# Kernel optimization log

Hardware: AMD Instinct MI355X
Metric: run time of the kernel (lower is better)

Reference implementation:

```python
import jax, jax.numpy as jnp
import numpy as np

N, E, MUL, HID = 50000, 400000, 32, 64


def setup_inputs() -> dict:
    key = jax.random.key(0)
    ks = jax.random.split(key, 16)
    inp = {
        'node_scalars': jax.random.normal(ks[0], (N, MUL), jnp.float32),
        'node_vectors': jax.random.normal(ks[1], (N, MUL, 3), jnp.float32),
        'sh': jax.random.normal(ks[2], (E, 4), jnp.float32),
        'norm': jax.random.uniform(ks[3], (E, 1), jnp.float32),
        'mlp_w1': jax.random.normal(ks[4], (1, HID), jnp.float32),
        'mlp_b1': jnp.zeros((HID,), jnp.float32),
        'mlp_w2': jax.random.normal(ks[5], (HID, HID), jnp.float32) / np.sqrt(HID),
        'mlp_b2': jnp.zeros((HID,), jnp.float32),
        'mlp_w3': jax.random.normal(ks[6], (HID, 4 * MUL), jnp.float32) / np.sqrt(HID),
        'mlp_b3': jnp.zeros((4 * MUL,), jnp.float32),
        'lin1_w_s': jax.random.normal(ks[7], (2 * MUL, 6 * MUL), jnp.float32),
        'lin1_w_v': jax.random.normal(ks[8], (2 * MUL, 2 * MUL), jnp.float32),
        'lin2_w_s': jax.random.normal(ks[9], (5 * MUL, MUL), jnp.float32),
        'lin2_w_v': jax.random.normal(ks[10], (3 * MUL, MUL), jnp.float32),
        'senders': jax.random.randint(ks[11], (E,), 0, N, jnp.int32),
        'receivers': jax.random.randint(ks[12], (E,), 0, N, jnp.int32),
    }
    return inp


def reference(node_scalars, node_vectors, sh, norm,
              mlp_w1, mlp_b1, mlp_w2, mlp_b2, mlp_w3, mlp_b3,
              lin1_w_s, lin1_w_v, lin2_w_s, lin2_w_v,
              senders, receivers):
    n = node_scalars.shape[0]
    y0, y1 = sh[:, :1], sh[:, 1:]                      # 0e SH [E,1], 1o SH [E,3]
    # ---- gather sender features ----
    s_e = node_scalars[senders]                         # [E,MUL]
    v_e = node_vectors[senders]                         # [E,MUL,3]
    # ---- CG tensor product (sh 0e+1o) x (MULx0e + MULx1o) -> 2MULx0e + 2MULx1o ----
    tp_s = jnp.concatenate([y0 * s_e,
                            jnp.einsum('ek,emk->em', y1, v_e) / jnp.sqrt(3.0)], axis=-1)   # [E,2MUL]
    tp_v = jnp.concatenate([y0[:, :, None] * v_e,
                            y1[:, None, :] * s_e[:, :, None]], axis=1)                      # [E,2MUL,3]
    # ---- MLP on edge norms -> one gating scalar per output irrep (4MUL) ----
    h = jax.nn.silu(norm @ mlp_w1 + mlp_b1)
    h = jax.nn.silu(h @ mlp_w2 + mlp_b2)
    scal = h @ mlp_w3 + mlp_b3                          # [E,4MUL]
    m2 = tp_s.shape[-1]
    tp_s = tp_s * scal[:, :m2]
    tp_v = tp_v * scal[:, m2:, None]
    # ---- scatter-mean into receivers ----
    cnt = jax.ops.segment_sum(jnp.ones((receivers.shape[0],), tp_s.dtype), receivers, num_segments=n)
    denom = jnp.maximum(cnt, 1.0)[:, None]
    agg_s = jax.ops.segment_sum(tp_s, receivers, num_segments=n) / denom                    # [N,2MUL]
    agg_v = jax.ops.segment_sum(tp_v, receivers, num_segments=n) / denom[:, :, None]        # [N,2MUL,3]
    # ---- equivariant Linear -> irreps + gate scalars ----
    x_s = agg_s @ lin1_w_s / jnp.sqrt(jnp.float32(agg_s.shape[-1]))                         # [N,6MUL]
    x_v = jnp.einsum('nmi,mo->noi', agg_v, lin1_w_v) / jnp.sqrt(jnp.float32(agg_v.shape[1]))# [N,2MUL,3]
    n_vec = x_v.shape[1]
    act_s = jax.nn.silu(x_s[:, : x_s.shape[-1] - n_vec])                                    # [N,4MUL]
    gates = jax.nn.sigmoid(x_s[:, x_s.shape[-1] - n_vec:])                                  # [N,2MUL]
    g_v = x_v * gates[:, :, None]
    # ---- concat skip + final Linear to output irreps (MULx0e + MULx1o) ----
    c_s = jnp.concatenate([act_s, node_scalars], axis=-1)                                   # [N,5MUL]
    c_v = jnp.concatenate([g_v, node_vectors], axis=1)                                      # [N,3MUL,3]
    o_s = c_s @ lin2_w_s / jnp.sqrt(jnp.float32(c_s.shape[-1]))                             # [N,MUL]
    o_v = jnp.einsum('nmi,mo->noi', c_v, lin2_w_v) / jnp.sqrt(jnp.float32(c_v.shape[1]))    # [N,MUL,3]
    return jnp.concatenate([o_s, o_v.reshape(o_v.shape[0], -1)], axis=-1)                   # [N,4MUL]
```

## Files before the change

### kernel.cpp

```cpp
#include <hip/hip_runtime.h>

#define NN 50000
#define NE 400000
#define NBINS 1024
#define NSBIN 512

#define RL1ST 0
#define RL1VT 12288
#define RL2S  16384
#define RL2V  21504
#define WTOT  24576

#define SLUT_N ((NBINS+1)*256)
#define INTS_N (3*NN + 1 + NE + 1024)
#define FIXED_FL ((size_t)WTOT + SLUT_N + INTS_N)

#define SCAN_B 196

#define S160 0.07905694150420949f
#define S96  0.10206207261596576f

__device__ __forceinline__ float sigf(float x){
  return __builtin_amdgcn_rcpf(1.0f + __expf(-x));
}
__device__ __forceinline__ float siluf(float x){ return x * sigf(x); }

__global__ __launch_bounds__(256) void convert_weights(
    const float* __restrict__ l1s, const float* __restrict__ l1v,
    const float* __restrict__ l2s, const float* __restrict__ l2v,
    float* __restrict__ wgt)
{
  int i = blockIdx.x*256 + threadIdx.x;
  if (i < 12288){ int o=i>>6, m=i&63; wgt[RL1ST + i] = l1s[m*192+o]; return; }
  if (i < 16384){ int t=i-12288; int o=t>>6, m=t&63; wgt[RL1VT + t] = l1v[m*64+o]; return; }
  if (i < 21504){ int t=i-16384; wgt[RL2S + t] = l2s[t]; return; }
  if (i < 24576){ int t=i-21504; wgt[RL2V + t] = l2v[t]; return; }
}

__global__ __launch_bounds__(128) void build_lut(
    const float* __restrict__ w1, const float* __restrict__ b1,
    const float* __restrict__ w2, const float* __restrict__ b2,
    const float* __restrict__ w3, const float* __restrict__ b3,
    float* __restrict__ slut)
{
  __shared__ float h1[64], h2[64], scal[128];
  int bin = blockIdx.x;
  float x = (float)bin / (float)NBINS;
  int t = threadIdx.x;
  if (t < 64) h1[t] = siluf(fmaf(x, w1[t], b1[t]));
  __syncthreads();
  if (t < 64){
    float a = b2[t];
    for (int k=0;k<64;k++) a = fmaf(h1[k], w2[k*64+t], a);
    h2[t] = siluf(a);
  }
  __syncthreads();
  {
    float a = b3[t];
    for (int k=0;k<64;k++) a = fmaf(h2[k], w3[k*128+t], a);
    scal[t] = a;
  }
  __syncthreads();
  for (int c=t; c<256; c+=128){
    int m=c>>3, q=c&7;
    int idx = (q==0)? m : (q==1)? (32+m) : (q<5)? (64+m) : (96+m);
    float v = scal[idx];
    if (q == 1) v *= 0.57735026918962576f;
    slut[(size_t)bin*256 + c] = v;
  }
}

__global__ __launch_bounds__(256) void count_kernel(
    const int* __restrict__ rcv, int* __restrict__ cnt)
{
  int e = blockIdx.x*256 + threadIdx.x;
  if (e < NE) atomicAdd(&cnt[rcv[e]], 1);
}

__global__ __launch_bounds__(256) void scan_a(
    const int* __restrict__ cnt, int* __restrict__ offs, int* __restrict__ bsum)
{
  __shared__ int sd[256];
  int tid = threadIdx.x;
  int i = blockIdx.x*256 + tid;
  int c = (i < NN) ? cnt[i] : 0;
  sd[tid] = c;
  __syncthreads();
  for (int off=1; off<256; off<<=1){
    int t = (tid >= off) ? sd[tid-off] : 0;
    __syncthreads();
    sd[tid] += t;
    __syncthreads();
  }
  if (i < NN) offs[i] = sd[tid] - c;
  if (tid == 255) bsum[blockIdx.x] = sd[255];
}

__global__ __launch_bounds__(256) void scan_b(
    const int* __restrict__ bsum, int* __restrict__ bbase, int* __restrict__ offs)
{
  __shared__ int sd[256];
  int tid = threadIdx.x;
  int v = (tid < SCAN_B) ? bsum[tid] : 0;
  sd[tid] = v;
  __syncthreads();
  for (int off=1; off<256; off<<=1){
    int t = (tid >= off) ? sd[tid-off] : 0;
    __syncthreads();
    sd[tid] += t;
    __syncthreads();
  }
  if (tid < SCAN_B) bbase[tid] = sd[tid] - v;
  if (tid == 255) offs[NN] = sd[255];
}

__global__ __launch_bounds__(256) void scan_c(
    const int* __restrict__ bbase, int* __restrict__ offs, int* __restrict__ curs)
{
  int i = blockIdx.x*256 + threadIdx.x;
  if (i < NN){
    int o = offs[i] + bbase[blockIdx.x];
    offs[i] = o;
    curs[i] = o;
  }
}

__global__ __launch_bounds__(256) void scatter_kernel(
    const int* __restrict__ rcv, int* __restrict__ curs, int* __restrict__ eids)
{
  int e = blockIdx.x*256 + threadIdx.x;
  if (e >= NE) return;
  int pos = atomicAdd(&curs[rcv[e]], 1);
  eids[pos] = e;
}

__global__ __launch_bounds__(256) void dhist_kernel(
    const int* __restrict__ offs, int* __restrict__ hist, int cn0, int cnn)
{
  __shared__ int lh[NSBIN];
  for (int j=threadIdx.x; j<NSBIN; j+=256) lh[j]=0;
  __syncthreads();
  int i = blockIdx.x*256 + threadIdx.x;
  if (i < cnn){
    int n = cn0 + i;
    int d = offs[n+1] - offs[n];
    int b = (d < NSBIN) ? (NSBIN-1-d) : 0;
    atomicAdd(&lh[b], 1);
  }
  __syncthreads();
  for (int j=threadIdx.x; j<NSBIN; j+=256){
    int v = lh[j];
    if (v) atomicAdd(&hist[j], v);
  }
}

__global__ __launch_bounds__(512) void dhist_scan(int* __restrict__ hist)
{
  __shared__ int sd[512];
  int t = threadIdx.x;
  int v = hist[t];
  sd[t] = v;
  __syncthreads();
  for (int off=1; off<512; off<<=1){
    int x = (t >= off) ? sd[t-off] : 0;
    __syncthreads();
    sd[t] += x;
    __syncthreads();
  }
  hist[t] = sd[t] - v;
}

__global__ __launch_bounds__(256) void dsort_kernel(
    const int* __restrict__ offs, int* __restrict__ hist,
    int* __restrict__ sorted, int cn0, int cnn)
{
  __shared__ int lh[NSBIN];
  __shared__ int lb[NSBIN];
  for (int j=threadIdx.x; j<NSBIN; j+=256) lh[j]=0;
  __syncthreads();
  int i = blockIdx.x*256 + threadIdx.x;
  int b = -1, rank = 0;
  if (i < cnn){
    int n = cn0 + i;
    int d = offs[n+1] - offs[n];
    b = (d < NSBIN) ? (NSBIN-1-d) : 0;
    rank = atomicAdd(&lh[b], 1);
  }
  __syncthreads();
  for (int j=threadIdx.x; j<NSBIN; j+=256){
    int v = lh[j];
    lb[j] = v ? atomicAdd(&hist[j], v) : 0;
  }
  __syncthreads();
  if (i < cnn) sorted[cn0 + lb[b] + rank] = cn0 + i;
}

__global__ __launch_bounds__(256) void edge_agg_kernel(
    const float* __restrict__ ns, const float* __restrict__ nv,
    const float* __restrict__ sh, const float* __restrict__ nrm,
    const int* __restrict__ snd,
    const int* __restrict__ offs, const int* __restrict__ eids,
    const int* __restrict__ sorted,
    const float* __restrict__ slut,
    float* __restrict__ agg, int cn0, int cnn)
{
  int wave = threadIdx.x >> 6;
  int lane = threadIdx.x & 63;
  int es = lane >> 5;
  int l  = lane & 31;
  int nls = blockIdx.x*4 + wave;
  if (nls >= cnn) return;
  int n = sorted[cn0 + nls];
  int p0 = offs[n], p1 = offs[n+1];
  const float4* slut4 = (const float4*)slut;
  float a0=0.f,a1=0.f,a2=0.f,a3=0.f,a4=0.f,a5=0.f,a6=0.f,a7=0.f;

  for (int base = p0; base < p1; base += 2){
    int p  = base + es;
    int pc = (p < p1) ? p : (p1 - 1);
    float ok = (p < p1) ? 1.0f : 0.0f;
    int e = eids[pc];
    int s = snd[e];
    float x = nrm[e];
    float4 y = *(const float4*)(sh + 4*e);

    float f = fminf(fmaxf(x*(float)NBINS, 0.0f), (float)NBINS - 0.001f);
    int b = (int)f;
    float tt = f - (float)b;
    const float4* Sp = slut4 + (size_t)b*64 + 2*l;
    float4 La = Sp[0];
    float4 Lb = Sp[1];
    float4 Lc = Sp[64];
    float4 Ld = Sp[65];

    float se = ns[(size_t)s*32 + l] * ok;
    const float* vp = nv + (size_t)s*96 + 3*l;
    float2 w = *(const float2*)vp;
    float v2 = vp[2];
    float v0 = w.x*ok, v1 = w.y*ok; v2 *= ok;

    float sc0 = fmaf(tt, Lc.x-La.x, La.x);
    float sc1 = fmaf(tt, Lc.y-La.y, La.y);
    float sc2 = fmaf(tt, Lc.z-La.z, La.z);
    float sc3 = fmaf(tt, Lc.w-La.w, La.w);
    float sc4 = fmaf(tt, Ld.x-Lb.x, Lb.x);
    float sc5 = fmaf(tt, Ld.y-Lb.y, Lb.y);
    float sc6 = fmaf(tt, Ld.z-Lb.z, Lb.z);
    float sc7 = fmaf(tt, Ld.w-Lb.w, Lb.w);

    float dot = fmaf(y.w, v2, fmaf(y.z, v1, y.y*v0));
    a0 = fmaf(y.x*se, sc0, a0);
    a1 = fmaf(dot,    sc1, a1);
    a2 = fmaf(y.x*v0, sc2, a2);
    a3 = fmaf(y.x*v1, sc3, a3);
    a4 = fmaf(y.x*v2, sc4, a4);
    a5 = fmaf(y.y*se, sc5, a5);
    a6 = fmaf(y.z*se, sc6, a6);
    a7 = fmaf(y.w*se, sc7, a7);
  }

  a0 += __shfl_xor(a0, 32); a1 += __shfl_xor(a1, 32);
  a2 += __shfl_xor(a2, 32); a3 += __shfl_xor(a3, 32);
  a4 += __shfl_xor(a4, 32); a5 += __shfl_xor(a5, 32);
  a6 += __shfl_xor(a6, 32); a7 += __shfl_xor(a7, 32);

  if (es == 0){
    int deg = p1 - p0;
    float inv = (deg > 0) ? __builtin_amdgcn_rcpf((float)deg) : 1.0f;
    float* ap = agg + (size_t)(n - cn0)*256;
    ap[l]       = a0*inv;
    ap[32+l]    = a1*inv;
    ap[64+l]    = a2*inv;
    ap[128+l]   = a3*inv;
    ap[192+l]   = a4*inv;
    ap[96+l]    = a5*inv;
    ap[160+l]   = a6*inv;
    ap[224+l]   = a7*inv;
  }
}

__global__ __launch_bounds__(256) __attribute__((amdgpu_waves_per_eu(3,8)))
void node_s_kernel(
    const float* __restrict__ ns, const float* __restrict__ wgt,
    const float* __restrict__ agg, int cn0, int cnn,
    float* __restrict__ out)
{
  __shared__ float red[3*64*33];
  int lane = threadIdx.x & 63, role = threadIdx.x >> 6;
  int ro = __builtin_amdgcn_readfirstlane(role);
  int nl = blockIdx.x*64 + lane;
  bool valid = (nl < cnn);
  int nls = valid ? nl : (cnn-1);
  int n = cn0 + nl;

  float aggs[64];
  float oacc[32];
  #pragma unroll
  for (int j=0;j<32;j++) oacc[j]=0.0f;

  {
    const float4* ar = (const float4*)(agg + (size_t)nls*256);
    #pragma unroll
    for (int g=0; g<16; g++){
      float4 v = ar[g];
      aggs[4*g+0]=v.x; aggs[4*g+1]=v.y; aggs[4*g+2]=v.z; aggs[4*g+3]=v.w;
    }
  }
  const float* l1sT = wgt + RL1ST + ro*32*64;
  const float* l2s  = wgt + RL2S;
  for (int t=0;t<32;t++){
    const float4* col = (const float4*)(l1sT + t*64);
    float d0=0,d1=0,d2=0,d3=0;
    #pragma unroll
    for (int j=0;j<16;j++){
      float4 c = col[j];
      d0 = fmaf(aggs[4*j+0], c.x, d0);
      d1 = fmaf(aggs[4*j+1], c.y, d1);
      d2 = fmaf(aggs[4*j+2], c.z, d2);
      d3 = fmaf(aggs[4*j+3], c.w, d3);
    }
    float act = siluf(((d0+d1)+(d2+d3))*0.125f);
    const float4* row = (const float4*)(l2s + (size_t)(ro*32 + t)*32);
    #pragma unroll
    for (int j=0;j<8;j++){
      float4 w = row[j];
      oacc[4*j+0] = fmaf(act, w.x, oacc[4*j+0]);
      oacc[4*j+1] = fmaf(act, w.y, oacc[4*j+1]);
      oacc[4*j+2] = fmaf(act, w.z, oacc[4*j+2]);
      oacc[4*j+3] = fmaf(act, w.w, oacc[4*j+3]);
    }
  }
  {
    const float4* sp = (const float4*)(ns + (size_t)(cn0+nls)*32 + ro*8);
    #pragma unroll
    for (int q4=0;q4<2;q4++){
      float4 v = sp[q4];
      float vv[4] = {v.x, v.y, v.z, v.w};
      #pragma unroll
      for (int u=0;u<4;u++){
        int q = ro*8 + q4*4 + u;
        const float4* row = (const float4*)(l2s + (size_t)(128+q)*32);
        #pragma unroll
        for (int j=0;j<8;j++){
          float4 w = row[j];
          oacc[4*j+0] = fmaf(vv[u], w.x, oacc[4*j+0]);
          oacc[4*j+1] = fmaf(vv[u], w.y, oacc[4*j+1]);
          oacc[4*j+2] = fmaf(vv[u], w.z, oacc[4*j+2]);
          oacc[4*j+3] = fmaf(vv[u], w.w, oacc[4*j+3]);
        }
      }
    }
  }

  if (role != 0){
    float* rp = red + (role-1)*(64*33) + lane*33;
    #pragma unroll
    for (int j=0;j<32;j++) rp[j] = oacc[j];
  }
  __syncthreads();
  if (role == 0 && valid){
    #pragma unroll
    for (int j=0;j<32;j++)
      oacc[j] += red[0*(64*33)+lane*33+j] + red[1*(64*33)+lane*33+j]
               + red[2*(64*33)+lane*33+j];
    float4* op = (float4*)(out + (size_t)n*128);
    #pragma unroll
    for (int j=0;j<8;j++){
      float4 o4;
      o4.x = oacc[4*j+0]*S160; o4.y = oacc[4*j+1]*S160;
      o4.z = oacc[4*j+2]*S160; o4.w = oacc[4*j+3]*S160;
      op[j] = o4;
    }
  }
}

__global__ __launch_bounds__(192) __attribute__((amdgpu_waves_per_eu(3,8)))
void node_v_kernel(
    const float* __restrict__ nv, const float* __restrict__ wgt,
    const float* __restrict__ agg, int cn0, int cnn,
    float* __restrict__ out)
{
  __shared__ float sw[64*97];
  int lane = threadIdx.x & 63, role = threadIdx.x >> 6;
  int ro = __builtin_amdgcn_readfirstlane(role);
  int nl = blockIdx.x*64 + lane;
  bool valid = (nl < cnn);
  int nls = valid ? nl : (cnn-1);
  const float* arow = agg + (size_t)nls*256;

  {
    float aggs[64];
    const float4* ar = (const float4*)arow;
    #pragma unroll
    for (int g=0; g<16; g++){
      float4 v = ar[g];
      aggs[4*g+0]=v.x; aggs[4*g+1]=v.y; aggs[4*g+2]=v.z; aggs[4*g+3]=v.w;
    }
    const float* l1g = wgt + RL1ST + 128*64;
    for (int o=ro; o<64; o+=3){
      const float4* col = (const float4*)(l1g + o*64);
      float d0=0,d1=0,d2=0,d3=0;
      #pragma unroll
      for (int j=0;j<16;j++){
        float4 c = col[j];
        d0 = fmaf(aggs[4*j+0], c.x, d0);
        d1 = fmaf(aggs[4*j+1], c.y, d1);
        d2 = fmaf(aggs[4*j+2], c.z, d2);
        d3 = fmaf(aggs[4*j+3], c.w, d3);
      }
      sw[o*64+lane] = sigf(((d0+d1)+(d2+d3))*0.125f);
    }
  }
  __syncthreads();

  int k = role;
  float aggv[64], oacc[32];
  #pragma unroll
  for (int j=0;j<32;j++) oacc[j]=0.0f;
  {
    const float4* av = (const float4*)(arow + 64 + 64*k);
    #pragma unroll
    for (int g=0; g<16; g++){
      float4 v = av[g];
      aggv[4*g+0]=v.x; aggv[4*g+1]=v.y; aggv[4*g+2]=v.z; aggv[4*g+3]=v.w;
    }
  }
  const float* l1vT = wgt + RL1VT;
  const float* l2v  = wgt + RL2V;
  for (int o=0;o<64;o++){
    const float4* col = (const float4*)(l1vT + o*64);
    float d0=0,d1=0,d2=0,d3=0;
    #pragma unroll
    for (int j=0;j<16;j++){
      float4 c = col[j];
      d0 = fmaf(aggv[4*j+0], c.x, d0);
      d1 = fmaf(aggv[4*j+1], c.y, d1);
      d2 = fmaf(aggv[4*j+2], c.z, d2);
      d3 = fmaf(aggv[4*j+3], c.w, d3);
    }
    float gv = (((d0+d1)+(d2+d3))*0.125f) * sw[o*64+lane];
    const float4* row = (const float4*)(l2v + (size_t)o*32);
    #pragma unroll
    for (int j=0;j<8;j++){
      float4 w = row[j];
      oacc[4*j+0] = fmaf(gv, w.x, oacc[4*j+0]);
      oacc[4*j+1] = fmaf(gv, w.y, oacc[4*j+1]);
      oacc[4*j+2] = fmaf(gv, w.z, oacc[4*j+2]);
      oacc[4*j+3] = fmaf(gv, w.w, oacc[4*j+3]);
    }
  }
  {
    const float* vp = nv + (size_t)(cn0+nls)*96 + k;
    #pragma unroll 8
    for (int q=0;q<32;q++){
      float a = vp[3*q];
      const float4* row = (const float4*)(l2v + (size_t)(64+q)*32);
      #pragma unroll
      for (int j=0;j<8;j++){
        float4 w = row[j];
        oacc[4*j+0] = fmaf(a, w.x, oacc[4*j+0]);
        oacc[4*j+1] = fmaf(a, w.y, oacc[4*j+1]);
        oacc[4*j+2] = fmaf(a, w.z, oacc[4*j+2]);
        oacc[4*j+3] = fmaf(a, w.w, oacc[4*j+3]);
      }
    }
  }

  __syncthreads();
  if (valid){
    #pragma unroll
    for (int j=0;j<32;j++) sw[lane*97 + 3*j + k] = oacc[j]*S96;
  }
  __syncthreads();
  int nb = blockIdx.x*64;
  #pragma unroll
  for (int r=0;r<8;r++){
    int F = r*192 + threadIdx.x;
    int i = F/24, j = F%24;
    if (nb + i < cnn){
      float4 o4;
      o4.x = sw[i*97 + 4*j + 0];
      o4.y = sw[i*97 + 4*j + 1];
      o4.z = sw[i*97 + 4*j + 2];
      o4.w = sw[i*97 + 4*j + 3];
      *(float4*)(out + (size_t)(cn0+nb+i)*128 + 32 + 4*j) = o4;
    }
  }
}

extern "C" void kernel_launch(void* const* d_in, const int* in_sizes, int n_in,
                              void* d_out, int out_size, void* d_ws, size_t ws_size,
                              hipStream_t stream) {
  const float* node_scalars = (const float*)d_in[0];
  const float* node_vectors = (const float*)d_in[1];
  const float* sh           = (const float*)d_in[2];
  const float* norm         = (const float*)d_in[3];
  const float* w1  = (const float*)d_in[4];
  const float* b1  = (const float*)d_in[5];
  const float* w2  = (const float*)d_in[6];
  const float* b2  = (const float*)d_in[7];
  const float* w3  = (const float*)d_in[8];
  const float* b3  = (const float*)d_in[9];
  const float* l1s = (const float*)d_in[10];
  const float* l1v = (const float*)d_in[11];
  const float* l2s = (const float*)d_in[12];
  const float* l2v = (const float*)d_in[13];
  const int* snd = (const int*)d_in[14];
  const int* rcv = (const int*)d_in[15];
  float* ws = (float*)d_ws;
  float* out = (float*)d_out;

  size_t ws_fl = ws_size / 4;
  if (ws_fl < FIXED_FL + 64*256) return;
  size_t aggcap = (ws_fl - FIXED_FL) / 256;
  int csize = (int)((aggcap < (size_t)NN) ? aggcap : (size_t)NN);
  int nchunks = (NN + csize - 1) / csize;

  float* wgt  = ws;
  float* slut = wgt + WTOT;
  int*   ib   = (int*)(slut + SLUT_N);
  int* offs   = ib;
  int* curs   = ib + NN + 1;
  int* eids   = ib + 2*NN + 1;
  int* sorted = ib + 2*NN + 1 + NE;
  int* cnt    = sorted;
  int* hist   = ib + 3*NN + 1 + NE;
  int* bsum   = hist + 512;
  int* bbase  = bsum + 256;
  float* agg  = (float*)(bbase + 256);

  hipMemsetAsync(cnt, 0, NN*sizeof(int), stream);

  convert_weights<<<(WTOT+255)/256, 256, 0, stream>>>(l1s, l1v, l2s, l2v, wgt);
  build_lut<<<NBINS+1, 128, 0, stream>>>(w1,b1,w2,b2,w3,b3, slut);

  count_kernel<<<(NE+255)/256, 256, 0, stream>>>(rcv, cnt);
  scan_a<<<SCAN_B, 256, 0, stream>>>(cnt, offs, bsum);
  scan_b<<<1, 256, 0, stream>>>(bsum, bbase, offs);
  scan_c<<<SCAN_B, 256, 0, stream>>>(bbase, offs, curs);
  scatter_kernel<<<(NE+255)/256, 256, 0, stream>>>(rcv, curs, eids);

  for (int ch = 0; ch < nchunks; ch++){
    int cn0 = ch * csize;
    int cnn = (NN - cn0 < csize) ? (NN - cn0) : csize;
    hipMemsetAsync(hist, 0, NSBIN*sizeof(int), stream);
    dhist_kernel<<<(cnn+255)/256, 256, 0, stream>>>(offs, hist, cn0, cnn);
    dhist_scan<<<1, 512, 0, stream>>>(hist);
    dsort_kernel<<<(cnn+255)/256, 256, 0, stream>>>(offs, hist, sorted, cn0, cnn);

    edge_agg_kernel<<<(cnn+3)/4, 256, 0, stream>>>(
        node_scalars, node_vectors, sh, norm, snd, offs, eids, sorted, slut,
        agg, cn0, cnn);
    node_s_kernel<<<(cnn+63)/64, 256, 0, stream>>>(
        node_scalars, wgt, agg, cn0, cnn, out);
    node_v_kernel<<<(cnn+63)/64, 192, 0, stream>>>(
        node_vectors, wgt, agg, cn0, cnn, out);
  }
}
```

Measured before the change: 354.2 us.

## Fuse node scalar and vector kernels into one 448-thread block kernel

Merges node_s_kernel and node_v_kernel into a single node_kernel where waves 0-3 handle the scalar path and waves 4-6 the vector path over the same 64 nodes. This removes one kernel launch per chunk and lets both paths share the agg rows in cache. The trade-off is larger per-block shared memory (red plus sw), changed occupancy bounds, and extra block-wide barriers that now make the scalar waves wait on the vector work. It also adds an unroll-2 pragma on the edge aggregation loop.

```diff
diff --git a/kernel.cpp b/kernel.cpp
--- a/kernel.cpp
+++ b/kernel.cpp
@@ -215,6 +215,7 @@
   const float4* slut4 = (const float4*)slut;
   float a0=0.f,a1=0.f,a2=0.f,a3=0.f,a4=0.f,a5=0.f,a6=0.f,a7=0.f;
 
+  #pragma unroll 2
   for (int base = p0; base < p1; base += 2){
     int p  = base + es;
     int pc = (p < p1) ? p : (p1 - 1);
@@ -279,126 +280,43 @@
   }
 }
 
-__global__ __launch_bounds__(256) __attribute__((amdgpu_waves_per_eu(3,8)))
-void node_s_kernel(
-    const float* __restrict__ ns, const float* __restrict__ wgt,
-    const float* __restrict__ agg, int cn0, int cnn,
-    float* __restrict__ out)
+__global__ __launch_bounds__(448) __attribute__((amdgpu_waves_per_eu(2,4)))
+void node_kernel(
+    const float* __restrict__ ns, const float* __restrict__ nv,
+    const float* __restrict__ wgt, const float* __restrict__ agg,
+    int cn0, int cnn, float* __restrict__ out)
 {
   __shared__ float red[3*64*33];
-  int lane = threadIdx.x & 63, role = threadIdx.x >> 6;
-  int ro = __builtin_amdgcn_readfirstlane(role);
+  __shared__ float sw[64*97];
+  int tid = threadIdx.x;
+  int wave = tid >> 6, lane = tid & 63;
+  bool isS = (wave < 4);
   int nl = blockIdx.x*64 + lane;
   bool valid = (nl < cnn);
   int nls = valid ? nl : (cnn-1);
   int n = cn0 + nl;
-
-  float aggs[64];
+  const float* arow = agg + (size_t)nls*256;
+  int kv = wave - 4;
+
   float oacc[32];
   #pragma unroll
   for (int j=0;j<32;j++) oacc[j]=0.0f;
 
-  {
-    const float4* ar = (const float4*)(agg + (size_t)nls*256);
-    #pragma unroll
-    for (int g=0; g<16; g++){
-      float4 v = ar[g];
-      aggs[4*g+0]=v.x; aggs[4*g+1]=v.y; aggs[4*g+2]=v.z; aggs[4*g+3]=v.w;
-    }
-  }
-  const float* l1sT = wgt + RL1ST + ro*32*64;
-  const float* l2s  = wgt + RL2S;
-  for (int t=0;t<32;t++){
-    const float4* col = (const float4*)(l1sT + t*64);
-    float d0=0,d1=0,d2=0,d3=0;
-    #pragma unroll
-    for (int j=0;j<16;j++){
-      float4 c = col[j];
-      d0 = fmaf(aggs[4*j+0], c.x, d0);
-      d1 = fmaf(aggs[4*j+1], c.y, d1);
-      d2 = fmaf(aggs[4*j+2], c.z, d2);
-      d3 = fmaf(aggs[4*j+3], c.w, d3);
-    }
-    float act = siluf(((d0+d1)+(d2+d3))*0.125f);
-    const float4* row = (const float4*)(l2s + (size_t)(ro*32 + t)*32);
-    #pragma unroll
-    for (int j=0;j<8;j++){
-      float4 w = row[j];
-      oacc[4*j+0] = fmaf(act, w.x, oacc[4*j+0]);
-      oacc[4*j+1] = fmaf(act, w.y, oacc[4*j+1]);
-      oacc[4*j+2] = fmaf(act, w.z, oacc[4*j+2]);
-      oacc[4*j+3] = fmaf(act, w.w, oacc[4*j+3]);
-    }
-  }
-  {
-    const float4* sp = (const float4*)(ns + (size_t)(cn0+nls)*32 + ro*8);
-    #pragma unroll
-    for (int q4=0;q4<2;q4++){
-      float4 v = sp[q4];
-      float vv[4] = {v.x, v.y, v.z, v.w};
-      #pragma unroll
-      for (int u=0;u<4;u++){
-        int q = ro*8 + q4*4 + u;
-        const float4* row = (const float4*)(l2s + (size_t)(128+q)*32);
-        #pragma unroll
-        for (int j=0;j<8;j++){
-          float4 w = row[j];
-          oacc[4*j+0] = fmaf(vv[u], w.x, oacc[4*j+0]);
-          oacc[4*j+1] = fmaf(vv[u], w.y, oacc[4*j+1]);
-          oacc[4*j+2] = fmaf(vv[u], w.z, oacc[4*j+2]);
-          oacc[4*j+3] = fmaf(vv[u], w.w, oacc[4*j+3]);
-        }
-      }
-    }
-  }
-
-  if (role != 0){
-    float* rp = red + (role-1)*(64*33) + lane*33;
-    #pragma unroll
-    for (int j=0;j<32;j++) rp[j] = oacc[j];
-  }
-  __syncthreads();
-  if (role == 0 && valid){
-    #pragma unroll
-    for (int j=0;j<32;j++)
-      oacc[j] += red[0*(64*33)+lane*33+j] + red[1*(64*33)+lane*33+j]
-               + red[2*(64*33)+lane*33+j];
-    float4* op = (float4*)(out + (size_t)n*128);
-    #pragma unroll
-    for (int j=0;j<8;j++){
-      float4 o4;
-      o4.x = oacc[4*j+0]*S160; o4.y = oacc[4*j+1]*S160;
-      o4.z = oacc[4*j+2]*S160; o4.w = oacc[4*j+3]*S160;
-      op[j] = o4;
-    }
-  }
-}
-
-__global__ __launch_bounds__(192) __attribute__((amdgpu_waves_per_eu(3,8)))
-void node_v_kernel(
-    const float* __restrict__ nv, const float* __restrict__ wgt,
-    const float* __restrict__ agg, int cn0, int cnn,
-    float* __restrict__ out)
-{
-  __shared__ float sw[64*97];
-  int lane = threadIdx.x & 63, role = threadIdx.x >> 6;
-  int ro = __builtin_amdgcn_readfirstlane(role);
-  int nl = blockIdx.x*64 + lane;
-  bool valid = (nl < cnn);
-  int nls = valid ? nl : (cnn-1);
-  const float* arow = agg + (size_t)nls*256;
-
-  {
+  if (isS){
+    int ro = __builtin_amdgcn_readfirstlane(wave);
     float aggs[64];
-    const float4* ar = (const float4*)arow;
-    #pragma unroll
-    for (int g=0; g<16; g++){
-      float4 v = ar[g];
-      aggs[4*g+0]=v.x; aggs[4*g+1]=v.y; aggs[4*g+2]=v.z; aggs[4*g+3]=v.w;
-    }
-    const float* l1g = wgt + RL1ST + 128*64;
-    for (int o=ro; o<64; o+=3){
-      const float4* col = (const float4*)(l1g + o*64);
+    {
+      const float4* ar = (const float4*)arow;
+      #pragma unroll
+      for (int g=0; g<16; g++){
+        float4 v = ar[g];
+        aggs[4*g+0]=v.x; aggs[4*g+1]=v.y; aggs[4*g+2]=v.z; aggs[4*g+3]=v.w;
+      }
+    }
+    const float* l1sT = wgt + RL1ST + ro*32*64;
+    const float* l2s  = wgt + RL2S;
+    for (int t=0;t<32;t++){
+      const float4* col = (const float4*)(l1sT + t*64);
       float d0=0,d1=0,d2=0,d3=0;
       #pragma unroll
       for (int j=0;j<16;j++){
@@ -408,74 +326,149 @@
         d2 = fmaf(aggs[4*j+2], c.z, d2);
         d3 = fmaf(aggs[4*j+3], c.w, d3);
       }
-      sw[o*64+lane] = sigf(((d0+d1)+(d2+d3))*0.125f);
-    }
-  }
-  __syncthreads();
-
-  int k = role;
-  float aggv[64], oacc[32];
-  #pragma unroll
-  for (int j=0;j<32;j++) oacc[j]=0.0f;
-  {
-    const float4* av = (const float4*)(arow + 64 + 64*k);
-    #pragma unroll
-    for (int g=0; g<16; g++){
-      float4 v = av[g];
-      aggv[4*g+0]=v.x; aggv[4*g+1]=v.y; aggv[4*g+2]=v.z; aggv[4*g+3]=v.w;
-    }
-  }
-  const float* l1vT = wgt + RL1VT;
-  const float* l2v  = wgt + RL2V;
-  for (int o=0;o<64;o++){
-    const float4* col = (const float4*)(l1vT + o*64);
-    float d0=0,d1=0,d2=0,d3=0;
-    #pragma unroll
-    for (int j=0;j<16;j++){
-      float4 c = col[j];
-      d0 = fmaf(aggv[4*j+0], c.x, d0);
-      d1 = fmaf(aggv[4*j+1], c.y, d1);
-      d2 = fmaf(aggv[4*j+2], c.z, d2);
-      d3 = fmaf(aggv[4*j+3], c.w, d3);
-    }
-    float gv = (((d0+d1)+(d2+d3))*0.125f) * sw[o*64+lane];
-    const float4* row = (const float4*)(l2v + (size_t)o*32);
-    #pragma unroll
-    for (int j=0;j<8;j++){
-      float4 w = row[j];
-      oacc[4*j+0] = fmaf(gv, w.x, oacc[4*j+0]);
-      oacc[4*j+1] = fmaf(gv, w.y, oacc[4*j+1]);
-      oacc[4*j+2] = fmaf(gv, w.z, oacc[4*j+2]);
-      oacc[4*j+3] = fmaf(gv, w.w, oacc[4*j+3]);
-    }
-  }
-  {
-    const float* vp = nv + (size_t)(cn0+nls)*96 + k;
-    #pragma unroll 8
-    for (int q=0;q<32;q++){
-      float a = vp[3*q];
-      const float4* row = (const float4*)(l2v + (size_t)(64+q)*32);
+      float act = siluf(((d0+d1)+(d2+d3))*0.125f);
+      const float4* row = (const float4*)(l2s + (size_t)(ro*32 + t)*32);
       #pragma unroll
       for (int j=0;j<8;j++){
         float4 w = row[j];
-        oacc[4*j+0] = fmaf(a, w.x, oacc[4*j+0]);
-        oacc[4*j+1] = fmaf(a, w.y, oacc[4*j+1]);
-        oacc[4*j+2] = fmaf(a, w.z, oacc[4*j+2]);
-        oacc[4*j+3] = fmaf(a, w.w, oacc[4*j+3]);
-      }
-    }
-  }
-
-  __syncthreads();
-  if (valid){
+        oacc[4*j+0] = fmaf(act, w.x, oacc[4*j+0]);
+        oacc[4*j+1] = fmaf(act, w.y, oacc[4*j+1]);
+        oacc[4*j+2] = fmaf(act, w.z, oacc[4*j+2]);
+        oacc[4*j+3] = fmaf(act, w.w, oacc[4*j+3]);
+      }
+    }
+    {
+      const float4* sp = (const float4*)(ns + (size_t)(cn0+nls)*32 + ro*8);
+      #pragma unroll
+      for (int q4=0;q4<2;q4++){
+        float4 v = sp[q4];
+        float vv[4] = {v.x, v.y, v.z, v.w};
+        #pragma unroll
+        for (int u=0;u<4;u++){
+          int q = ro*8 + q4*4 + u;
+          const float4* row = (const float4*)(l2s + (size_t)(128+q)*32);
+          #pragma unroll
+          for (int j=0;j<8;j++){
+            float4 w = row[j];
+            oacc[4*j+0] = fmaf(vv[u], w.x, oacc[4*j+0]);
+            oacc[4*j+1] = fmaf(vv[u], w.y, oacc[4*j+1]);
+            oacc[4*j+2] = fmaf(vv[u], w.z, oacc[4*j+2]);
+            oacc[4*j+3] = fmaf(vv[u], w.w, oacc[4*j+3]);
+          }
+        }
+      }
+    }
+    if (wave != 0){
+      float* rp = red + (wave-1)*(64*33) + lane*33;
+      #pragma unroll
+      for (int j=0;j<32;j++) rp[j] = oacc[j];
+    }
+  } else {
+    int ro = __builtin_amdgcn_readfirstlane(kv);
+    float aggs[64];
+    {
+      const float4* ar = (const float4*)arow;
+      #pragma unroll
+      for (int g=0; g<16; g++){
+        float4 v = ar[g];
+        aggs[4*g+0]=v.x; aggs[4*g+1]=v.y; aggs[4*g+2]=v.z; aggs[4*g+3]=v.w;
+      }
+    }
+    const float* l1g = wgt + RL1ST + 128*64;
+    for (int o=ro; o<64; o+=3){
+      const float4* col = (const float4*)(l1g + o*64);
+      float d0=0,d1=0,d2=0,d3=0;
+      #pragma unroll
+      for (int j=0;j<16;j++){
+        float4 c = col[j];
+        d0 = fmaf(aggs[4*j+0], c.x, d0);
+        d1 = fmaf(aggs[4*j+1], c.y, d1);
+        d2 = fmaf(aggs[4*j+2], c.z, d2);
+        d3 = fmaf(aggs[4*j+3], c.w, d3);
+      }
+      sw[o*64+lane] = sigf(((d0+d1)+(d2+d3))*0.125f);
+    }
+  }
+  __syncthreads();
+
+  if (isS){
+    if (wave == 0 && valid){
+      #pragma unroll
+      for (int j=0;j<32;j++)
+        oacc[j] += red[0*(64*33)+lane*33+j] + red[1*(64*33)+lane*33+j]
+                 + red[2*(64*33)+lane*33+j];
+      float4* op = (float4*)(out + (size_t)n*128);
+      #pragma unroll
+      for (int j=0;j<8;j++){
+        float4 o4;
+        o4.x = oacc[4*j+0]*S160; o4.y = oacc[4*j+1]*S160;
+        o4.z = oacc[4*j+2]*S160; o4.w = oacc[4*j+3]*S160;
+        op[j] = o4;
+      }
+    }
+  } else {
+    float aggv[64];
     #pragma unroll
-    for (int j=0;j<32;j++) sw[lane*97 + 3*j + k] = oacc[j]*S96;
-  }
-  __syncthreads();
+    for (int j=0;j<32;j++) oacc[j]=0.0f;
+    {
+      const float4* av = (const float4*)(arow + 64 + 64*kv);
+      #pragma unroll
+      for (int g=0; g<16; g++){
+        float4 v = av[g];
+        aggv[4*g+0]=v.x; aggv[4*g+1]=v.y; aggv[4*g+2]=v.z; aggv[4*g+3]=v.w;
+      }
+    }
+    const float* l1vT = wgt + RL1VT;
+    const float* l2v  = wgt + RL2V;
+    for (int o=0;o<64;o++){
+      const float4* col = (const float4*)(l1vT + o*64);
+      float d0=0,d1=0,d2=0,d3=0;
+      #pragma unroll
+      for (int j=0;j<16;j++){
+        float4 c = col[j];
+        d0 = fmaf(aggv[4*j+0], c.x, d0);
+        d1 = fmaf(aggv[4*j+1], c.y, d1);
+        d2 = fmaf(aggv[4*j+2], c.z, d2);
+        d3 = fmaf(aggv[4*j+3], c.w, d3);
+      }
+      float gv = (((d0+d1)+(d2+d3))*0.125f) * sw[o*64+lane];
+      const float4* row = (const float4*)(l2v + (size_t)o*32);
+      #pragma unroll
+      for (int j=0;j<8;j++){
+        float4 w = row[j];
+        oacc[4*j+0] = fmaf(gv, w.x, oacc[4*j+0]);
+        oacc[4*j+1] = fmaf(gv, w.y, oacc[4*j+1]);
+        oacc[4*j+2] = fmaf(gv, w.z, oacc[4*j+2]);
+        oacc[4*j+3] = fmaf(gv, w.w, oacc[4*j+3]);
+      }
+    }
+    {
+      const float* vp = nv + (size_t)(cn0+nls)*96 + kv;
+      #pragma unroll 8
+      for (int q=0;q<32;q++){
+        float a = vp[3*q];
+        const float4* row = (const float4*)(l2v + (size_t)(64+q)*32);
+        #pragma unroll
+        for (int j=0;j<8;j++){
+          float4 w = row[j];
+          oacc[4*j+0] = fmaf(a, w.x, oacc[4*j+0]);
+          oacc[4*j+1] = fmaf(a, w.y, oacc[4*j+1]);
+          oacc[4*j+2] = fmaf(a, w.z, oacc[4*j+2]);
+          oacc[4*j+3] = fmaf(a, w.w, oacc[4*j+3]);
+        }
+      }
+    }
+  }
+  __syncthreads();
+
+  if (!isS && valid){
+    #pragma unroll
+    for (int j=0;j<32;j++) sw[lane*97 + 3*j + kv] = oacc[j]*S96;
+  }
+  __syncthreads();
+
   int nb = blockIdx.x*64;
-  #pragma unroll
-  for (int r=0;r<8;r++){
-    int F = r*192 + threadIdx.x;
+  for (int F = tid; F < 1536; F += 448){
     int i = F/24, j = F%24;
     if (nb + i < cnn){
       float4 o4;
@@ -551,9 +544,7 @@
     edge_agg_kernel<<<(cnn+3)/4, 256, 0, stream>>>(
         node_scalars, node_vectors, sh, norm, snd, offs, eids, sorted, slut,
         agg, cn0, cnn);
-    node_s_kernel<<<(cnn+63)/64, 256, 0, stream>>>(
-        node_scalars, wgt, agg, cn0, cnn, out);
-    node_v_kernel<<<(cnn+63)/64, 192, 0, stream>>>(
-        node_vectors, wgt, agg, cn0, cnn, out);
-  }
-}
+    node_kernel<<<(cnn+63)/64, 448, 0, stream>>>(
+        node_scalars, node_vectors, wgt, agg, cn0, cnn, out);
+  }
+}
```

After: 401.4 us. 1.13x slower.
